# Kernel tuning notes

Measured on AMD Instinct MI355X. Metric: run time of the kernel, lower is better.

Reference implementation:

```python
import jax, jax.numpy as jnp
import numpy as np

HEADS = 8
LN_EPS = 1e-5

def setup_inputs() -> dict:
    key = jax.random.key(0)
    ks = jax.random.split(key, 12)
    B, T, N, D = 4, 24, 400, 256
    s = 1.0 / np.sqrt(D)
    x = jax.random.normal(ks[0], (B, T, N, D), dtype=jnp.float32)
    adj = jax.random.uniform(ks[1], (B, T, N, N), dtype=jnp.float32)
    Wq = jax.random.uniform(ks[2], (D, D), jnp.float32, -s, s)
    bq = jax.random.uniform(ks[3], (D,), jnp.float32, -s, s)
    Wk = jax.random.uniform(ks[4], (D, D), jnp.float32, -s, s)
    bk = jax.random.uniform(ks[5], (D,), jnp.float32, -s, s)
    Wv = jax.random.uniform(ks[6], (D, D), jnp.float32, -s, s)
    bv = jax.random.uniform(ks[7], (D,), jnp.float32, -s, s)
    gamma = jnp.ones((D,), jnp.float32)
    beta = jnp.zeros((D,), jnp.float32)
    return {"x": x, "adj": adj, "Wq": Wq, "bq": bq, "Wk": Wk, "bk": bk,
            "Wv": Wv, "bv": bv, "gamma": gamma, "beta": beta}

def reference(x, adj, Wq, bq, Wk, bk, Wv, bv, gamma, beta):
    B, T, N, D = x.shape
    H = HEADS
    hd = D // H
    # QKV projections (torch Linear: x @ W.T + b)
    q = (x @ Wq.T + bq).reshape(B, T, N, H, hd)
    k = (x @ Wk.T + bk).reshape(B, T, N, H, hd)
    v = (x @ Wv.T + bv).reshape(B, T, N, H, hd)
    # scores [B,T,H,N,N], scaled then multiplicatively masked by adj
    a = jnp.einsum('btnhd,btmhd->bthnm', q, k) / jnp.sqrt(jnp.float32(hd))
    a = a * adj[:, :, None, :, :]
    a = jax.nn.softmax(a, axis=-1)
    h = jnp.einsum('bthnm,btmhd->btnhd', a, v).reshape(B, T, N, D)
    # dropout is identity in eval; residual + LayerNorm
    y = h + x
    mu = jnp.mean(y, axis=-1, keepdims=True)
    var = jnp.mean((y - mu) ** 2, axis=-1, keepdims=True)
    return (y - mu) * jax.lax.rsqrt(var + LN_EPS) * gamma + beta
```

## Files before the change

### kernel.cpp

```cpp
#include <hip/hip_runtime.h>
#include <cstdint>
#include <cstddef>

typedef unsigned short u16;
typedef __attribute__((ext_vector_type(8))) __bf16 bf16x8;
typedef __attribute__((ext_vector_type(4))) float f32x4;
typedef __attribute__((ext_vector_type(8))) u16 u16x8;
typedef __attribute__((ext_vector_type(4))) u16 u16x4;

#define MTOT   38400
#define DMODEL 256
#define NQKV   768
#define NN     400
#define NBT    96
#define SCALE  0.17677669529663687f

__device__ __forceinline__ u16 f2b(float f){
  __bf16 b = (__bf16)f;
  return __builtin_bit_cast(u16, b);
}

__device__ __forceinline__ void g2l16(const void* g, void* l){
  __builtin_amdgcn_global_load_lds(
      (const __attribute__((address_space(1))) unsigned int*)g,
      (__attribute__((address_space(3))) unsigned int*)l,
      16, 0, 0);
}

__global__ __launch_bounds__(256) void cast_x_kernel(const float* __restrict__ x,
                                                     u16* __restrict__ xb, int n8){
  int i = blockIdx.x * 256 + threadIdx.x;
  if (i >= n8) return;
  const f32x4* xp = (const f32x4*)x;
  f32x4 a = xp[2*i], b = xp[2*i+1];
  u16x8 o;
  o[0]=f2b(a[0]); o[1]=f2b(a[1]); o[2]=f2b(a[2]); o[3]=f2b(a[3]);
  o[4]=f2b(b[0]); o[5]=f2b(b[1]); o[6]=f2b(b[2]); o[7]=f2b(b[3]);
  ((u16x8*)xb)[i] = o;
}

__global__ __launch_bounds__(256) void prep_w_kernel(
    const float* __restrict__ wq, const float* __restrict__ wk, const float* __restrict__ wv,
    const float* __restrict__ bq, const float* __restrict__ bk, const float* __restrict__ bv,
    u16* __restrict__ wqkv, float* __restrict__ bqkv){
  int i = blockIdx.x * 256 + threadIdx.x;
  int g = i >> 14;
  int rem = (i & 16383) * 4;
  const float* w = (g == 0) ? wq : ((g == 1) ? wk : wv);
  float sc = (g == 0) ? SCALE : 1.0f;
  f32x4 v = *(const f32x4*)(w + rem);
  u16x4 o; o[0]=f2b(v[0]*sc); o[1]=f2b(v[1]*sc); o[2]=f2b(v[2]*sc); o[3]=f2b(v[3]*sc);
  *(u16x4*)(wqkv + (size_t)i*4) = o;
  if (i < NQKV) bqkv[i] = (i < 256) ? bq[i]*SCALE : ((i < 512) ? bk[i-256] : bv[i-512]);
}

__global__ __launch_bounds__(256,2) void gemm_qkv_kernel(
    const u16* __restrict__ xb, const u16* __restrict__ wqkv,
    const float* __restrict__ bqkv, u16* __restrict__ qkv){
  __shared__ u16 a_lds[128*64];
  __shared__ u16 b_lds[128*64];
  const int tid = threadIdx.x, lane = tid & 63, wave = tid >> 6;
  const int bn = blockIdx.x % 6, bm = blockIdx.x / 6;
  const int m0 = bm*128, n0 = bn*128;
  const int wm = (wave>>1)*64, wn = (wave&1)*64;
  const int lr = lane & 15, lk = lane >> 4;
  f32x4 acc[4][4] = {};
  for (int k0 = 0; k0 < 256; k0 += 64){
    #pragma unroll
    for (int i = 0; i < 4; ++i){
      int off  = (wave*4 + i)*1024 + lane*16;
      int row  = off >> 7;
      int colb = off & 127;
      int scolb = colb ^ ((row & 7) << 4);
      g2l16(xb   + (size_t)(m0+row)*256 + k0 + (scolb>>1), (char*)a_lds + (size_t)(wave*4+i)*1024);
      g2l16(wqkv + (size_t)(n0+row)*256 + k0 + (scolb>>1), (char*)b_lds + (size_t)(wave*4+i)*1024);
    }
    __syncthreads();
    #pragma unroll
    for (int sub = 0; sub < 2; ++sub){
      bf16x8 af[4], bfr[4];
      #pragma unroll
      for (int i = 0; i < 4; ++i){
        int ra = wm + i*16 + lr;
        af[i]  = *(const bf16x8*)((const char*)a_lds + ra*128 + ((sub*64 + lk*16) ^ ((ra&7)<<4)));
        int rb = wn + i*16 + lr;
        bfr[i] = *(const bf16x8*)((const char*)b_lds + rb*128 + ((sub*64 + lk*16) ^ ((rb&7)<<4)));
      }
      #pragma unroll
      for (int i = 0; i < 4; ++i)
        #pragma unroll
        for (int j = 0; j < 4; ++j)
          acc[i][j] = __builtin_amdgcn_mfma_f32_16x16x32_bf16(af[i], bfr[j], acc[i][j], 0, 0, 0);
    }
    __syncthreads();
  }
  #pragma unroll
  for (int j = 0; j < 4; ++j){
    int n = n0 + wn + j*16 + lr;
    float bias = bqkv[n];
    #pragma unroll
    for (int i = 0; i < 4; ++i){
      int mb = m0 + wm + i*16 + lk*4;
      #pragma unroll
      for (int r = 0; r < 4; ++r)
        qkv[(size_t)(mb + r)*NQKV + n] = f2b(acc[i][j][r] + bias);
    }
  }
}

#define VT_STRIDE 424
#define PW_STRIDE 40
#define K_BYTES   25600
#define VT_BYTES  27136

__global__ __launch_bounds__(256,2) void attn_kernel(
    const u16* __restrict__ qkv, const float* __restrict__ adj, float* __restrict__ hout){
  __shared__ __align__(16) char smem[62976];
  u16* vT    = (u16*)(smem + K_BYTES);
  u16* p_all = (u16*)(smem + K_BYTES + VT_BYTES);
  const int tid = threadIdx.x, lane = tid & 63, wave = tid >> 6;
  const int h = blockIdx.x / NBT, bt = blockIdx.x % NBT;
  const int lq = lane & 15, lk = lane >> 4;
  const u16* qkvbt = qkv + (size_t)bt*NN*NQKV + h*32;

  {
    const u16* kbase = qkvbt + 256;
    int rsub = lane >> 2;
    int colb = (lane & 3) * 16;
    for (int c = wave; c < 25; c += 4){
      int row  = c*16 + rsub;
      int scol = colb ^ ((row & 3) << 4);
      g2l16(kbase + (size_t)row*NQKV + (scol >> 1), smem + c*1024);
    }
  }
  for (int c = tid; c < 1600; c += 256){
    int row = c >> 2, cc = (c & 3)*8;
    u16x8 v = *(const u16x8*)(qkvbt + 512 + (size_t)row*NQKV + cc);
    #pragma unroll
    for (int e = 0; e < 8; ++e) vT[(cc+e)*VT_STRIDE + row] = v[e];
  }
  for (int i = tid; i < 32*16; i += 256) vT[(i>>4)*VT_STRIDE + 400 + (i&15)] = 0;
  __syncthreads();

  const float* adjbt = adj + (size_t)bt*NN*NN;
  u16* pw = p_all + wave*(2*16*PW_STRIDE);
  const f32x4 z = {0.f, 0.f, 0.f, 0.f};

  for (int t25 = wave; t25 < 25; t25 += 4){
    const int q0 = t25*16;
    bf16x8 qf = *(const bf16x8*)(qkvbt + (size_t)(q0 + lq)*NQKV + lk*8);
    f32x4 s[25];
    #pragma unroll
    for (int kt = 0; kt < 25; ++kt){
      int row = kt*16 + lq;
      bf16x8 kf = *(const bf16x8*)((const char*)smem + row*64 + ((lk*16) ^ ((row & 3) << 4)));
      s[kt] = __builtin_amdgcn_mfma_f32_16x16x32_bf16(kf, qf, z, 0, 0, 0);
    }
    const float* arow = adjbt + (size_t)(q0 + lq)*NN + lk*4;
    #pragma unroll
    for (int kt = 0; kt < 25; ++kt){
      f32x4 a = *(const f32x4*)(arow + kt*16);
      s[kt] *= a;
    }
    f32x4 mv = s[0];
    #pragma unroll
    for (int kt = 1; kt < 25; ++kt){
      mv[0]=fmaxf(mv[0],s[kt][0]); mv[1]=fmaxf(mv[1],s[kt][1]);
      mv[2]=fmaxf(mv[2],s[kt][2]); mv[3]=fmaxf(mv[3],s[kt][3]);
    }
    float m = fmaxf(fmaxf(mv[0],mv[1]), fmaxf(mv[2],mv[3]));
    m = fmaxf(m, __shfl_xor(m, 16)); m = fmaxf(m, __shfl_xor(m, 32));
    f32x4 sv = z;
    #pragma unroll
    for (int kt = 0; kt < 25; ++kt){
      #pragma unroll
      for (int j = 0; j < 4; ++j){
        float e = __expf(s[kt][j] - m);
        s[kt][j] = e; sv[j] += e;
      }
    }
    float sum = (sv[0]+sv[1]) + (sv[2]+sv[3]);
    sum += __shfl_xor(sum, 16); sum += __shfl_xor(sum, 32);
    float inv = 1.0f / sum;
    f32x4 o0 = z, o1 = z;
    #pragma unroll
    for (int w = 0; w < 13; ++w){
      u16* buf = pw + (w & 1)*(16*PW_STRIDE);
      u16x4 pk0, pk1;
      #pragma unroll
      for (int j = 0; j < 4; ++j) pk0[j] = f2b(s[2*w][j]);
      if (w < 12){
        #pragma unroll
        for (int j = 0; j < 4; ++j) pk1[j] = f2b(s[2*w+1][j]);
      } else {
        pk1[0]=0; pk1[1]=0; pk1[2]=0; pk1[3]=0;
      }
      *(u16x4*)(buf + lq*PW_STRIDE + lk*4)      = pk0;
      *(u16x4*)(buf + lq*PW_STRIDE + 16 + lk*4) = pk1;
      bf16x8 pf = *(const bf16x8*)((const char*)buf + lq*80 + lk*16);
      bf16x8 v0 = *(const bf16x8*)((const char*)vT + (size_t)lq*848      + w*64 + lk*16);
      bf16x8 v1 = *(const bf16x8*)((const char*)vT + (size_t)(16+lq)*848 + w*64 + lk*16);
      o0 = __builtin_amdgcn_mfma_f32_16x16x32_bf16(pf, v0, o0, 0, 0, 0);
      o1 = __builtin_amdgcn_mfma_f32_16x16x32_bf16(pf, v1, o1, 0, 0, 0);
    }
    float* orow = hout + (size_t)(bt*NN + q0)*DMODEL + h*32;
    #pragma unroll
    for (int r = 0; r < 4; ++r){
      float invq = __shfl(inv, lk*4 + r);
      orow[(lk*4 + r)*DMODEL + lq]      = o0[r]*invq;
      orow[(lk*4 + r)*DMODEL + 16 + lq] = o1[r]*invq;
    }
  }
}

__global__ __launch_bounds__(256) void resid_ln_kernel(
    const float* __restrict__ hbuf, const float* __restrict__ x,
    const float* __restrict__ gamma, const float* __restrict__ beta,
    float* __restrict__ out){
  const int wave = threadIdx.x >> 6, lane = threadIdx.x & 63;
  const int row = blockIdx.x*4 + wave;
  const f32x4* hp = (const f32x4*)(hbuf + (size_t)row*DMODEL);
  const f32x4* xp = (const f32x4*)(x    + (size_t)row*DMODEL);
  f32x4 y = hp[lane] + xp[lane];
  float s = y[0] + y[1] + y[2] + y[3];
  s += __shfl_xor(s, 1);  s += __shfl_xor(s, 2);  s += __shfl_xor(s, 4);
  s += __shfl_xor(s, 8);  s += __shfl_xor(s, 16); s += __shfl_xor(s, 32);
  float mu = s * (1.0f/256.0f);
  f32x4 d = y - mu;
  float vs = d[0]*d[0] + d[1]*d[1] + d[2]*d[2] + d[3]*d[3];
  vs += __shfl_xor(vs, 1);  vs += __shfl_xor(vs, 2);  vs += __shfl_xor(vs, 4);
  vs += __shfl_xor(vs, 8);  vs += __shfl_xor(vs, 16); vs += __shfl_xor(vs, 32);
  float rs = rsqrtf(vs * (1.0f/256.0f) + 1e-5f);
  f32x4 g = ((const f32x4*)gamma)[lane];
  f32x4 b = ((const f32x4*)beta)[lane];
  f32x4 o = d*rs*g + b;
  ((f32x4*)(out + (size_t)row*DMODEL))[lane] = o;
}

extern "C" void kernel_launch(void* const* d_in, const int* in_sizes, int n_in,
                              void* d_out, int out_size, void* d_ws, size_t ws_size,
                              hipStream_t stream){
  const float* x     = (const float*)d_in[0];
  const float* adj   = (const float*)d_in[1];
  const float* Wq    = (const float*)d_in[2];
  const float* bq    = (const float*)d_in[3];
  const float* Wk    = (const float*)d_in[4];
  const float* bk    = (const float*)d_in[5];
  const float* Wv    = (const float*)d_in[6];
  const float* bv    = (const float*)d_in[7];
  const float* gamma = (const float*)d_in[8];
  const float* beta  = (const float*)d_in[9];
  float* out = (float*)d_out;
  char* ws = (char*)d_ws;

  u16*   xb   = (u16*)  (ws + 0);
  u16*   wqkv = (u16*)  (ws + 19660800);
  float* bqkv = (float*)(ws + 20054016);
  u16*   qkv  = (u16*)  (ws + 20057088);
  float* hbuf = (float*)(ws + 79039488);

  cast_x_kernel<<<4800, 256, 0, stream>>>(x, xb, 9830400/8);
  prep_w_kernel<<<192, 256, 0, stream>>>(Wq, Wk, Wv, bq, bk, bv, wqkv, bqkv);
  gemm_qkv_kernel<<<1800, 256, 0, stream>>>(xb, wqkv, bqkv, qkv);
  attn_kernel<<<768, 256, 0, stream>>>(qkv, adj, hbuf);
  resid_ln_kernel<<<9600, 256, 0, stream>>>(hbuf, x, gamma, beta, out);
}
```

Measured before the change: 251.8 us.

## Double-buffer QKV GEMM loads and move V transpose to separate kernel

The QKV GEMM now double-buffers its LDS tiles, prefetching the next K slice with async global-to-LDS loads and waiting on vmcnt before each barrier, so loads overlap the MFMA work. The V transpose moves out of the attention kernel into a new vt_prep kernel that writes a padded, transposed V to global memory. The attention kernel then reads V fragments straight from global memory, which cuts its LDS use enough to allow 3 blocks per CU. The cost is an extra launch, an extra round trip of V through global memory, and uncached global loads in the PV inner loop; xb and hbuf now share a workspace region, which relies on xb being dead before attention writes.

```diff
diff --git a/kernel.cpp b/kernel.cpp
--- a/kernel.cpp
+++ b/kernel.cpp
@@ -57,34 +57,48 @@
 __global__ __launch_bounds__(256,2) void gemm_qkv_kernel(
     const u16* __restrict__ xb, const u16* __restrict__ wqkv,
     const float* __restrict__ bqkv, u16* __restrict__ qkv){
-  __shared__ u16 a_lds[128*64];
-  __shared__ u16 b_lds[128*64];
+  __shared__ u16 a_lds[2][128*64];
+  __shared__ u16 b_lds[2][128*64];
   const int tid = threadIdx.x, lane = tid & 63, wave = tid >> 6;
   const int bn = blockIdx.x % 6, bm = blockIdx.x / 6;
   const int m0 = bm*128, n0 = bn*128;
   const int wm = (wave>>1)*64, wn = (wave&1)*64;
   const int lr = lane & 15, lk = lane >> 4;
   f32x4 acc[4][4] = {};
-  for (int k0 = 0; k0 < 256; k0 += 64){
+
+  auto stage = [&](int buf, int k0){
     #pragma unroll
     for (int i = 0; i < 4; ++i){
       int off  = (wave*4 + i)*1024 + lane*16;
       int row  = off >> 7;
       int colb = off & 127;
       int scolb = colb ^ ((row & 7) << 4);
-      g2l16(xb   + (size_t)(m0+row)*256 + k0 + (scolb>>1), (char*)a_lds + (size_t)(wave*4+i)*1024);
-      g2l16(wqkv + (size_t)(n0+row)*256 + k0 + (scolb>>1), (char*)b_lds + (size_t)(wave*4+i)*1024);
-    }
-    __syncthreads();
+      g2l16(xb   + (size_t)(m0+row)*256 + k0 + (scolb>>1), (char*)a_lds[buf] + (wave*4+i)*1024);
+      g2l16(wqkv + (size_t)(n0+row)*256 + k0 + (scolb>>1), (char*)b_lds[buf] + (wave*4+i)*1024);
+    }
+  };
+
+  stage(0, 0);
+  #pragma unroll
+  for (int ks = 0; ks < 4; ++ks){
+    if (ks < 3){
+      stage((ks+1)&1, (ks+1)*64);
+      asm volatile("s_waitcnt vmcnt(8)" ::: "memory");
+    } else {
+      asm volatile("s_waitcnt vmcnt(0)" ::: "memory");
+    }
+    __builtin_amdgcn_s_barrier();
+    const char* al = (const char*)a_lds[ks&1];
+    const char* bl = (const char*)b_lds[ks&1];
     #pragma unroll
     for (int sub = 0; sub < 2; ++sub){
       bf16x8 af[4], bfr[4];
       #pragma unroll
       for (int i = 0; i < 4; ++i){
         int ra = wm + i*16 + lr;
-        af[i]  = *(const bf16x8*)((const char*)a_lds + ra*128 + ((sub*64 + lk*16) ^ ((ra&7)<<4)));
+        af[i]  = *(const bf16x8*)(al + ra*128 + ((sub*64 + lk*16) ^ ((ra&7)<<4)));
         int rb = wn + i*16 + lr;
-        bfr[i] = *(const bf16x8*)((const char*)b_lds + rb*128 + ((sub*64 + lk*16) ^ ((rb&7)<<4)));
+        bfr[i] = *(const bf16x8*)(bl + rb*128 + ((sub*64 + lk*16) ^ ((rb&7)<<4)));
       }
       #pragma unroll
       for (int i = 0; i < 4; ++i)
@@ -92,7 +106,7 @@
         for (int j = 0; j < 4; ++j)
           acc[i][j] = __builtin_amdgcn_mfma_f32_16x16x32_bf16(af[i], bfr[j], acc[i][j], 0, 0, 0);
     }
-    __syncthreads();
+    __builtin_amdgcn_s_barrier();
   }
   #pragma unroll
   for (int j = 0; j < 4; ++j){
@@ -108,20 +122,39 @@
   }
 }
 
-#define VT_STRIDE 424
+__global__ __launch_bounds__(256) void vt_prep_kernel(const u16* __restrict__ qkv,
+                                                      u16* __restrict__ vtg){
+  const int bh = blockIdx.x, bt = bh >> 3, h = bh & 7;
+  const u16* vsrc = qkv + (size_t)bt*NN*NQKV + 512 + h*32;
+  u16* dst = vtg + (size_t)bh*32*416;
+  for (int idx = threadIdx.x; idx < 32*52; idx += 256){
+    int d = idx / 52, j = idx % 52;
+    int k0 = j*8;
+    u16x8 o;
+    if (k0 < 400){
+      #pragma unroll
+      for (int e = 0; e < 8; ++e) o[e] = vsrc[(size_t)(k0+e)*NQKV + d];
+    } else {
+      #pragma unroll
+      for (int e = 0; e < 8; ++e) o[e] = 0;
+    }
+    *(u16x8*)(dst + d*416 + k0) = o;
+  }
+}
+
 #define PW_STRIDE 40
 #define K_BYTES   25600
-#define VT_BYTES  27136
-
-__global__ __launch_bounds__(256,2) void attn_kernel(
-    const u16* __restrict__ qkv, const float* __restrict__ adj, float* __restrict__ hout){
-  __shared__ __align__(16) char smem[62976];
-  u16* vT    = (u16*)(smem + K_BYTES);
-  u16* p_all = (u16*)(smem + K_BYTES + VT_BYTES);
+
+__global__ __launch_bounds__(256,3) void attn_kernel(
+    const u16* __restrict__ qkv, const u16* __restrict__ vtg,
+    const float* __restrict__ adj, float* __restrict__ hout){
+  __shared__ __align__(16) char smem[35840];
+  u16* p_all = (u16*)(smem + K_BYTES);
   const int tid = threadIdx.x, lane = tid & 63, wave = tid >> 6;
   const int h = blockIdx.x / NBT, bt = blockIdx.x % NBT;
   const int lq = lane & 15, lk = lane >> 4;
   const u16* qkvbt = qkv + (size_t)bt*NN*NQKV + h*32;
+  const u16* vth   = vtg + (size_t)(bt*8 + h)*32*416;
 
   {
     const u16* kbase = qkvbt + 256;
@@ -133,13 +166,6 @@
       g2l16(kbase + (size_t)row*NQKV + (scol >> 1), smem + c*1024);
     }
   }
-  for (int c = tid; c < 1600; c += 256){
-    int row = c >> 2, cc = (c & 3)*8;
-    u16x8 v = *(const u16x8*)(qkvbt + 512 + (size_t)row*NQKV + cc);
-    #pragma unroll
-    for (int e = 0; e < 8; ++e) vT[(cc+e)*VT_STRIDE + row] = v[e];
-  }
-  for (int i = tid; i < 32*16; i += 256) vT[(i>>4)*VT_STRIDE + 400 + (i&15)] = 0;
   __syncthreads();
 
   const float* adjbt = adj + (size_t)bt*NN*NN;
@@ -198,8 +224,8 @@
       *(u16x4*)(buf + lq*PW_STRIDE + lk*4)      = pk0;
       *(u16x4*)(buf + lq*PW_STRIDE + 16 + lk*4) = pk1;
       bf16x8 pf = *(const bf16x8*)((const char*)buf + lq*80 + lk*16);
-      bf16x8 v0 = *(const bf16x8*)((const char*)vT + (size_t)lq*848      + w*64 + lk*16);
-      bf16x8 v1 = *(const bf16x8*)((const char*)vT + (size_t)(16+lq)*848 + w*64 + lk*16);
+      bf16x8 v0 = *(const bf16x8*)(vth + (size_t)lq*416      + w*32 + lk*8);
+      bf16x8 v1 = *(const bf16x8*)(vth + (size_t)(16+lq)*416 + w*32 + lk*8);
       o0 = __builtin_amdgcn_mfma_f32_16x16x32_bf16(pf, v0, o0, 0, 0, 0);
       o1 = __builtin_amdgcn_mfma_f32_16x16x32_bf16(pf, v1, o1, 0, 0, 0);
     }
@@ -253,15 +279,17 @@
   float* out = (float*)d_out;
   char* ws = (char*)d_ws;
 
-  u16*   xb   = (u16*)  (ws + 0);
-  u16*   wqkv = (u16*)  (ws + 19660800);
-  float* bqkv = (float*)(ws + 20054016);
-  u16*   qkv  = (u16*)  (ws + 20057088);
-  float* hbuf = (float*)(ws + 79039488);
+  u16*   vtg  = (u16*)  (ws + 0);
+  u16*   wqkv = (u16*)  (ws + 20447232);
+  float* bqkv = (float*)(ws + 20840448);
+  u16*   qkv  = (u16*)  (ws + 20843520);
+  float* hbuf = (float*)(ws + 79825920);
+  u16*   xb   = (u16*)  (ws + 79825920);
 
   cast_x_kernel<<<4800, 256, 0, stream>>>(x, xb, 9830400/8);
   prep_w_kernel<<<192, 256, 0, stream>>>(Wq, Wk, Wv, bq, bk, bv, wqkv, bqkv);
   gemm_qkv_kernel<<<1800, 256, 0, stream>>>(xb, wqkv, bqkv, qkv);
-  attn_kernel<<<768, 256, 0, stream>>>(qkv, adj, hbuf);
+  vt_prep_kernel<<<768, 256, 0, stream>>>(qkv, vtg);
+  attn_kernel<<<768, 256, 0, stream>>>(qkv, vtg, adj, hbuf);
   resid_ln_kernel<<<9600, 256, 0, stream>>>(hbuf, x, gamma, beta, out);
 }
```

After: 418.6 us. 1.66x slower.
